# Kernel optimization log

Measured on AMD Instinct MI355X. Metric: run time of the kernel, lower is better.

## Reference

```python
import jax, jax.numpy as jnp
import numpy as np

N, M, D_IN, D_TXT, D_OUT, H = 4096, 1024, 512, 512, 512, 8
DH = D_OUT // H


def positional_encoding(n, dim):
    # Matches PositionalEncoding: freq = exp((arange(dim//2)/dim)*ln(10000)),
    # x = pos/freq -> [L, dim//2], interleave (sin, cos) pairs -> [L, dim].
    pos = jnp.arange(n, dtype=jnp.float32)
    freq = jnp.exp((jnp.arange(dim // 2, dtype=jnp.float32) / dim) * jnp.log(jnp.float32(10000.0)))
    x = pos[:, None] / freq  # [L, dim//2]
    pe = jnp.stack((jnp.sin(x), jnp.cos(x)), axis=-1)  # [L, dim//2, 2]
    return pe.reshape(n, dim)


def setup_inputs() -> dict:
    key = jax.random.key(0)
    k1, k2, k3, k4, k5, k6 = jax.random.split(key, 6)
    s = 0.02
    return {
        "video_features": jax.random.normal(k1, (N, D_IN), dtype=jnp.float32),
        "text_features": jax.random.normal(k2, (M, D_TXT), dtype=jnp.float32),
        "Wq": jax.random.normal(k3, (H, D_IN, DH), dtype=jnp.float32) * s,
        "Wk": jax.random.normal(k4, (H, D_TXT, DH), dtype=jnp.float32) * s,
        "Wv": jax.random.normal(k5, (H, D_TXT, DH), dtype=jnp.float32) * s,
        "Wout": jax.random.normal(k6, (D_OUT, D_IN), dtype=jnp.float32) * s,
    }


def reference(video_features, text_features, Wq, Wk, Wv, Wout):
    # Batched over heads instead of the original per-head Python loop (same math).
    Q = jnp.einsum('nd,hde->hne', video_features, Wq)   # [H, N, DH]
    K = jnp.einsum('md,hde->hme', text_features, Wk)    # [H, M, DH]
    V = jnp.einsum('md,hde->hme', text_features, Wv)    # [H, M, DH]
    energies = jnp.einsum('hne,hme->hnm', Q, K)         # no scaling in original
    att = jax.nn.softmax(energies, axis=-1)             # dropout omitted (eval mode)
    y = jnp.einsum('hnm,hme->hne', att, V)              # [H, N, DH]
    y = jnp.transpose(y, (1, 0, 2)).reshape(video_features.shape[0], -1)  # concat heads
    y = y @ Wout                                        # [N, D_IN]
    y = y + positional_encoding(y.shape[0], y.shape[1])
    return y
```

## Files before the change

kernel.cpp:

```cpp
#include <hip/hip_runtime.h>
#include <hip/hip_bf16.h>
#include <math.h>

#define N_TOK 4096
#define M_TOK 1024
#define DMODEL 512
#define NHEAD 8
#define DHEAD 64

typedef __attribute__((ext_vector_type(8))) short short8;
typedef __attribute__((ext_vector_type(4))) float f32x4;
typedef __attribute__((ext_vector_type(4))) float float4v;
typedef __attribute__((ext_vector_type(2))) float float2v;

static __device__ __forceinline__ short f2bf(float f) {
    union { float f; unsigned u; } v; v.f = f;
    unsigned r = v.u + 0x7fffu + ((v.u >> 16) & 1u);
    return (short)(r >> 16);
}

#define GLOAD_LDS16(g, l) __builtin_amdgcn_global_load_lds( \
    (const __attribute__((address_space(1))) void*)(g), \
    (__attribute__((address_space(3))) void*)(l), 16, 0, 0)

__global__ void pack_kernel(const float* __restrict__ xv, const float* __restrict__ xt,
                            const float* __restrict__ wq, const float* __restrict__ wk,
                            const float* __restrict__ wv, const float* __restrict__ wo,
                            short* __restrict__ xvb, short* __restrict__ xtb,
                            short* __restrict__ wqb, short* __restrict__ wkb,
                            short* __restrict__ wvb, short* __restrict__ wob,
                            float* __restrict__ pe) {
    int idx = blockIdx.x * 256 + threadIdx.x;
    int stride = gridDim.x * 256;
    const int CXV = N_TOK * DMODEL / 8;
    const int CXT = M_TOK * DMODEL / 8;
    const int NW  = DMODEL * DMODEL;
    const int NPE = N_TOK * (DMODEL / 2);
    for (int c = idx; c < CXV; c += stride) {
        float4v f0 = *(const float4v*)&xv[c * 8];
        float4v f1 = *(const float4v*)&xv[c * 8 + 4];
        short8 o;
        #pragma unroll
        for (int j = 0; j < 4; j++) { o[j] = f2bf(f0[j]); o[j + 4] = f2bf(f1[j]); }
        *(short8*)&xvb[c * 8] = o;
    }
    for (int c = idx; c < CXT; c += stride) {
        float4v f0 = *(const float4v*)&xt[c * 8];
        float4v f1 = *(const float4v*)&xt[c * 8 + 4];
        short8 o;
        #pragma unroll
        for (int j = 0; j < 4; j++) { o[j] = f2bf(f0[j]); o[j + 4] = f2bf(f1[j]); }
        *(short8*)&xtb[c * 8] = o;
    }
    for (int i = idx; i < NW; i += stride) {
        int n = i >> 9;
        int k = i & 511;
        int h = n >> 6, e = n & 63;
        int src = h * (DMODEL * DHEAD) + k * DHEAD + e;
        wqb[i] = f2bf(wq[src]);
        wkb[i] = f2bf(wk[src]);
        wvb[i] = f2bf(wv[src]);
        wob[i] = f2bf(wo[k * DMODEL + n]);
    }
    for (int i = idx; i < NPE; i += stride) {
        int row = i >> 8;
        int p = i & 255;
        float fr = __expf(-(float)p * (9.210340371976184f / 512.0f));
        float x = (float)row * fr;
        float s, c;
        __sincosf(x, &s, &c);
        float2v sc; sc[0] = s; sc[1] = c;
        *(float2v*)&pe[(size_t)row * DMODEL + p * 2] = sc;
    }
}

template<typename EPI>
static __device__ __forceinline__ void gemm_body(const short* __restrict__ A,
                                                 const short* __restrict__ BT,
                                                 int m0, int n0, EPI epi) {
    __shared__ __align__(16) short As[64][72];
    __shared__ __align__(16) short Bs[64][72];
    int t = threadIdx.x;
    int lane = t & 63, w = t >> 6;
    int wr = w >> 1, wc = w & 1;
    int l15 = lane & 15, g = lane >> 4;

    int row = t >> 2, c0 = (t & 3) * 16;
    const short* gA = A + (size_t)(m0 + row) * DMODEL + c0;
    const short* gB = BT + (size_t)(n0 + row) * DMODEL + c0;

    short8 ra0 = *(const short8*)gA;
    short8 ra1 = *(const short8*)(gA + 8);
    short8 rb0 = *(const short8*)gB;
    short8 rb1 = *(const short8*)(gB + 8);

    f32x4 acc[2][2] = {};
    #pragma unroll
    for (int step = 0; step < DMODEL / 64; ++step) {
        *(short8*)&As[row][c0]     = ra0;
        *(short8*)&As[row][c0 + 8] = ra1;
        *(short8*)&Bs[row][c0]     = rb0;
        *(short8*)&Bs[row][c0 + 8] = rb1;
        __syncthreads();
        if (step < DMODEL / 64 - 1) {
            gA += 64; gB += 64;
            ra0 = *(const short8*)gA;
            ra1 = *(const short8*)(gA + 8);
            rb0 = *(const short8*)gB;
            rb1 = *(const short8*)(gB + 8);
        }
        #pragma unroll
        for (int ks = 0; ks < 2; ks++) {
            short8 a[2], b[2];
            #pragma unroll
            for (int fr = 0; fr < 2; fr++) a[fr] = *(short8*)&As[wr * 32 + fr * 16 + l15][ks * 32 + g * 8];
            #pragma unroll
            for (int fc = 0; fc < 2; fc++) b[fc] = *(short8*)&Bs[wc * 32 + fc * 16 + l15][ks * 32 + g * 8];
            #pragma unroll
            for (int fr = 0; fr < 2; fr++)
                #pragma unroll
                for (int fc = 0; fc < 2; fc++)
                    acc[fr][fc] = __builtin_amdgcn_mfma_f32_16x16x32_bf16(a[fr], b[fc], acc[fr][fc], 0, 0, 0);
        }
        __syncthreads();
    }
    #pragma unroll
    for (int fr = 0; fr < 2; fr++)
        #pragma unroll
        for (int fc = 0; fc < 2; fc++)
            #pragma unroll
            for (int r = 0; r < 4; r++) {
                int orow = m0 + wr * 32 + fr * 16 + g * 4 + r;
                int ocol = n0 + wc * 32 + fc * 16 + l15;
                epi(orow, ocol, acc[fr][fc][r]);
            }
}

__global__ __launch_bounds__(256) void gemmQKV(const short* __restrict__ xvb,
                                               const short* __restrict__ xtb,
                                               const short* __restrict__ wqb,
                                               const short* __restrict__ wkb,
                                               const short* __restrict__ wvb,
                                               short* __restrict__ qb,
                                               short* __restrict__ kbm,
                                               short* __restrict__ vbt) {
    int bx = blockIdx.x;
    int n0 = blockIdx.y * 64;
    if (bx < 64) {
        short* C = qb;
        gemm_body(xvb, wqb, bx * 64, n0,
                  [&](int row, int col, float v) { C[(size_t)row * DMODEL + col] = f2bf(v); });
    } else if (bx < 80) {
        short* C = kbm;
        gemm_body(xtb, wkb, (bx - 64) * 64, n0,
                  [&](int row, int col, float v) { C[(size_t)row * DMODEL + col] = f2bf(v); });
    } else {
        short* C = vbt;
        gemm_body(xtb, wvb, (bx - 80) * 64, n0,
                  [&](int row, int col, float v) { C[(size_t)col * M_TOK + row] = f2bf(v); });
    }
}

__global__ __launch_bounds__(256) void gemmOut(const short* __restrict__ A,
                                               const short* __restrict__ BT,
                                               const float* __restrict__ pe,
                                               float* __restrict__ Cout) {
    gemm_body(A, BT, blockIdx.x * 64, blockIdx.y * 64,
              [&](int row, int col, float v) {
                  size_t o = (size_t)row * DMODEL + col;
                  Cout[o] = v + pe[o];
              });
}

__global__ __launch_bounds__(256) void attn_kernel(const short* __restrict__ Qb,
                                                   const short* __restrict__ Kb,
                                                   const short* __restrict__ VbT,
                                                   short* __restrict__ Yb) {
    __shared__ __align__(16) short Ks[2][64][64];
    __shared__ __align__(16) short Vs[2][64][64];
    __shared__ __align__(16) short Ps[4][16][72];

    int bid = blockIdx.x;
    int h = bid & 7;
    int qx = bid >> 3;
    int n0 = qx * 64;
    int t = threadIdx.x;
    int lane = t & 63, w = t >> 6;
    int l15 = lane & 15, g = lane >> 4;

    const short* Kh  = Kb + h * DHEAD;
    const short* VhT = VbT + (h * DHEAD) * M_TOK;

    int srow = (lane >> 3);
    int sgran = (lane & 7) ^ srow;
    const short* gK0 = Kh + (size_t)(w * 16 + srow) * DMODEL + sgran * 8;
    const short* gV0 = VhT + (size_t)(w * 16 + srow) * M_TOK + sgran * 8;

    const short* qrow = Qb + (size_t)(n0 + w * 16 + l15) * DMODEL + h * DHEAD;
    short8 qa0 = *(const short8*)(qrow + g * 8);
    short8 qa1 = *(const short8*)(qrow + 32 + g * 8);

    f32x4 acc[4] = {};
    f32x4 rsum = {};
    int sx = l15 & 7;

    {
        GLOAD_LDS16(gK0,                 &Ks[0][w * 16][0]);
        GLOAD_LDS16(gK0 + 8 * DMODEL,    &Ks[0][w * 16 + 8][0]);
        GLOAD_LDS16(gV0,                 &Vs[0][w * 16][0]);
        GLOAD_LDS16(gV0 + 8 * M_TOK,     &Vs[0][w * 16 + 8][0]);
    }
    __syncthreads();

    int buf = 0;
    for (int it = 0; it < 16; ++it) {
        if (it < 15) {
            int key0 = (it + 1) * 64;
            GLOAD_LDS16(gK0 + (size_t)key0 * DMODEL,             &Ks[buf ^ 1][w * 16][0]);
            GLOAD_LDS16(gK0 + (size_t)(key0 + 8) * DMODEL,       &Ks[buf ^ 1][w * 16 + 8][0]);
            GLOAD_LDS16(gV0 + key0,                              &Vs[buf ^ 1][w * 16][0]);
            GLOAD_LDS16(gV0 + key0 + 8 * M_TOK,                  &Vs[buf ^ 1][w * 16 + 8][0]);
        }
        #pragma unroll
        for (int kt = 0; kt < 4; kt++) {
            short8 kf0 = *(short8*)&Ks[buf][kt * 16 + l15][((g) ^ sx) * 8];
            short8 kf1 = *(short8*)&Ks[buf][kt * 16 + l15][((4 + g) ^ sx) * 8];
            f32x4 e = {};
            e = __builtin_amdgcn_mfma_f32_16x16x32_bf16(qa0, kf0, e, 0, 0, 0);
            e = __builtin_amdgcn_mfma_f32_16x16x32_bf16(qa1, kf1, e, 0, 0, 0);
            #pragma unroll
            for (int r = 0; r < 4; r++) {
                float p = exp2f(e[r] * 1.44269504f);
                rsum[r] += p;
                Ps[w][g * 4 + r][kt * 16 + l15] = f2bf(p);
            }
        }
        #pragma unroll
        for (int kb2 = 0; kb2 < 2; kb2++) {
            short8 pa = *(short8*)&Ps[w][l15][kb2 * 32 + g * 8];
            #pragma unroll
            for (int nt = 0; nt < 4; nt++) {
                short8 vf = *(short8*)&Vs[buf][nt * 16 + l15][((kb2 * 4 + g) ^ sx) * 8];
                acc[nt] = __builtin_amdgcn_mfma_f32_16x16x32_bf16(pa, vf, acc[nt], 0, 0, 0);
            }
        }
        __syncthreads();
        buf ^= 1;
    }

    #pragma unroll
    for (int r = 0; r < 4; r++) {
        float s = rsum[r];
        s += __shfl_xor(s, 1);
        s += __shfl_xor(s, 2);
        s += __shfl_xor(s, 4);
        s += __shfl_xor(s, 8);
        rsum[r] = s;
    }

    #pragma unroll
    for (int nt = 0; nt < 4; nt++)
        #pragma unroll
        for (int r = 0; r < 4; r++) {
            float y = acc[nt][r] / rsum[r];
            Yb[(size_t)(n0 + w * 16 + g * 4 + r) * DMODEL + h * DHEAD + nt * 16 + l15] = f2bf(y);
        }
}

extern "C" void kernel_launch(void* const* d_in, const int* in_sizes, int n_in,
                              void* d_out, int out_size, void* d_ws, size_t ws_size,
                              hipStream_t stream) {
    const float* xv = (const float*)d_in[0];
    const float* xt = (const float*)d_in[1];
    const float* wq = (const float*)d_in[2];
    const float* wk = (const float*)d_in[3];
    const float* wv = (const float*)d_in[4];
    const float* wo = (const float*)d_in[5];

    short* xvb = (short*)d_ws;
    short* xtb = xvb + N_TOK * DMODEL;
    short* wqb = xtb + M_TOK * DMODEL;
    short* wkb = wqb + DMODEL * DMODEL;
    short* wvb = wkb + DMODEL * DMODEL;
    short* wob = wvb + DMODEL * DMODEL;
    short* qb  = wob + DMODEL * DMODEL;
    short* kbm = qb  + N_TOK * DMODEL;
    short* vbt = kbm + M_TOK * DMODEL;
    short* yb  = vbt + M_TOK * DMODEL;
    float* pe  = (float*)(yb + N_TOK * DMODEL);

    pack_kernel<<<1024, 256, 0, stream>>>(xv, xt, wq, wk, wv, wo,
                                          xvb, xtb, wqb, wkb, wvb, wob, pe);
    gemmQKV<<<dim3(96, 8), 256, 0, stream>>>(xvb, xtb, wqb, wkb, wvb, qb, kbm, vbt);
    attn_kernel<<<512, 256, 0, stream>>>(qb, kbm, vbt, yb);
    gemmOut<<<dim3(64, 8), 256, 0, stream>>>(yb, wob, pe, (float*)d_out);
}
```

Measured before the change: 62.65 us.

## Fuse QKV, attention and output GEMMs into persistent kernel with grid barriers

Replaces three separate launches (QKV GEMM, attention, output GEMM) with a single 512-block kernel that runs each stage in turn, separated by a software grid barrier built on global atomics, with shared memory reused through a union. The positional encoding is now computed inline in the output GEMM epilogue rather than being materialised by the pack kernel and read back. This removes launch gaps and the PE write/read traffic, but it depends on all 512 blocks being co-resident for the barrier. It also loses parallelism in the QKV stage, where half the blocks compute two tiles.

```diff
diff --git a/kernel.cpp b/kernel.cpp
--- a/kernel.cpp
+++ b/kernel.cpp
@@ -7,11 +7,11 @@
 #define DMODEL 512
 #define NHEAD 8
 #define DHEAD 64
+#define NBLK 512
 
 typedef __attribute__((ext_vector_type(8))) short short8;
 typedef __attribute__((ext_vector_type(4))) float f32x4;
 typedef __attribute__((ext_vector_type(4))) float float4v;
-typedef __attribute__((ext_vector_type(2))) float float2v;
 
 static __device__ __forceinline__ short f2bf(float f) {
     union { float f; unsigned u; } v; v.f = f;
@@ -22,6 +22,29 @@
 #define GLOAD_LDS16(g, l) __builtin_amdgcn_global_load_lds( \
     (const __attribute__((address_space(1))) void*)(g), \
     (__attribute__((address_space(3))) void*)(l), 16, 0, 0)
+
+struct SMemG { short As[64][72]; short Bs[64][72]; };
+struct SMemA { short Ks[2][64][64]; short Vs[2][64][64]; short Ps[4][16][72]; };
+union SMemU { SMemG g; SMemA a; };
+
+static __device__ __forceinline__ void gridbar(unsigned* cnt, unsigned* gen) {
+    __syncthreads();
+    if (threadIdx.x == 0) {
+        __threadfence();
+        unsigned g = __hip_atomic_load(gen, __ATOMIC_RELAXED, __HIP_MEMORY_SCOPE_AGENT);
+        if (__hip_atomic_fetch_add(cnt, 1u, __ATOMIC_ACQ_REL, __HIP_MEMORY_SCOPE_AGENT) == NBLK - 1u) {
+            __hip_atomic_store(cnt, 0u, __ATOMIC_RELAXED, __HIP_MEMORY_SCOPE_AGENT);
+            __hip_atomic_store(gen, g + 1u, __ATOMIC_RELEASE, __HIP_MEMORY_SCOPE_AGENT);
+        } else {
+            unsigned cur;
+            do {
+                __builtin_amdgcn_s_sleep(2);
+                cur = __hip_atomic_load(gen, __ATOMIC_ACQUIRE, __HIP_MEMORY_SCOPE_AGENT);
+            } while (cur == g);
+        }
+    }
+    __syncthreads();
+}
 
 __global__ void pack_kernel(const float* __restrict__ xv, const float* __restrict__ xt,
                             const float* __restrict__ wq, const float* __restrict__ wk,
@@ -29,13 +52,13 @@
                             short* __restrict__ xvb, short* __restrict__ xtb,
                             short* __restrict__ wqb, short* __restrict__ wkb,
                             short* __restrict__ wvb, short* __restrict__ wob,
-                            float* __restrict__ pe) {
+                            unsigned* __restrict__ bar) {
     int idx = blockIdx.x * 256 + threadIdx.x;
     int stride = gridDim.x * 256;
+    if (idx == 0) { bar[0] = 0u; bar[1] = 0u; }
     const int CXV = N_TOK * DMODEL / 8;
     const int CXT = M_TOK * DMODEL / 8;
     const int NW  = DMODEL * DMODEL;
-    const int NPE = N_TOK * (DMODEL / 2);
     for (int c = idx; c < CXV; c += stride) {
         float4v f0 = *(const float4v*)&xv[c * 8];
         float4v f1 = *(const float4v*)&xv[c * 8 + 4];
@@ -62,24 +85,13 @@
         wvb[i] = f2bf(wv[src]);
         wob[i] = f2bf(wo[k * DMODEL + n]);
     }
-    for (int i = idx; i < NPE; i += stride) {
-        int row = i >> 8;
-        int p = i & 255;
-        float fr = __expf(-(float)p * (9.210340371976184f / 512.0f));
-        float x = (float)row * fr;
-        float s, c;
-        __sincosf(x, &s, &c);
-        float2v sc; sc[0] = s; sc[1] = c;
-        *(float2v*)&pe[(size_t)row * DMODEL + p * 2] = sc;
-    }
 }
 
 template<typename EPI>
-static __device__ __forceinline__ void gemm_body(const short* __restrict__ A,
+static __device__ __forceinline__ void gemm_body(SMemG& sm,
+                                                 const short* __restrict__ A,
                                                  const short* __restrict__ BT,
                                                  int m0, int n0, EPI epi) {
-    __shared__ __align__(16) short As[64][72];
-    __shared__ __align__(16) short Bs[64][72];
     int t = threadIdx.x;
     int lane = t & 63, w = t >> 6;
     int wr = w >> 1, wc = w & 1;
@@ -97,10 +109,10 @@
     f32x4 acc[2][2] = {};
     #pragma unroll
     for (int step = 0; step < DMODEL / 64; ++step) {
-        *(short8*)&As[row][c0]     = ra0;
-        *(short8*)&As[row][c0 + 8] = ra1;
-        *(short8*)&Bs[row][c0]     = rb0;
-        *(short8*)&Bs[row][c0 + 8] = rb1;
+        *(short8*)&sm.As[row][c0]     = ra0;
+        *(short8*)&sm.As[row][c0 + 8] = ra1;
+        *(short8*)&sm.Bs[row][c0]     = rb0;
+        *(short8*)&sm.Bs[row][c0 + 8] = rb1;
         __syncthreads();
         if (step < DMODEL / 64 - 1) {
             gA += 64; gB += 64;
@@ -113,9 +125,9 @@
         for (int ks = 0; ks < 2; ks++) {
             short8 a[2], b[2];
             #pragma unroll
-            for (int fr = 0; fr < 2; fr++) a[fr] = *(short8*)&As[wr * 32 + fr * 16 + l15][ks * 32 + g * 8];
-            #pragma unroll
-            for (int fc = 0; fc < 2; fc++) b[fc] = *(short8*)&Bs[wc * 32 + fc * 16 + l15][ks * 32 + g * 8];
+            for (int fr = 0; fr < 2; fr++) a[fr] = *(short8*)&sm.As[wr * 32 + fr * 16 + l15][ks * 32 + g * 8];
+            #pragma unroll
+            for (int fc = 0; fc < 2; fc++) b[fc] = *(short8*)&sm.Bs[wc * 32 + fc * 16 + l15][ks * 32 + g * 8];
             #pragma unroll
             for (int fr = 0; fr < 2; fr++)
                 #pragma unroll
@@ -136,54 +148,32 @@
             }
 }
 
-__global__ __launch_bounds__(256) void gemmQKV(const short* __restrict__ xvb,
-                                               const short* __restrict__ xtb,
-                                               const short* __restrict__ wqb,
-                                               const short* __restrict__ wkb,
-                                               const short* __restrict__ wvb,
-                                               short* __restrict__ qb,
-                                               short* __restrict__ kbm,
-                                               short* __restrict__ vbt) {
-    int bx = blockIdx.x;
-    int n0 = blockIdx.y * 64;
-    if (bx < 64) {
-        short* C = qb;
-        gemm_body(xvb, wqb, bx * 64, n0,
-                  [&](int row, int col, float v) { C[(size_t)row * DMODEL + col] = f2bf(v); });
-    } else if (bx < 80) {
-        short* C = kbm;
-        gemm_body(xtb, wkb, (bx - 64) * 64, n0,
-                  [&](int row, int col, float v) { C[(size_t)row * DMODEL + col] = f2bf(v); });
+static __device__ __forceinline__ void qkv_tile(SMemG& sm, int tile,
+                                                const short* xvb, const short* xtb,
+                                                const short* wqb, const short* wkb,
+                                                const short* wvb,
+                                                short* qb, short* kbm, short* vbt) {
+    if (tile < 512) {
+        gemm_body(sm, xvb, wqb, (tile >> 3) * 64, (tile & 7) * 64,
+                  [&](int row, int col, float v) { qb[(size_t)row * DMODEL + col] = f2bf(v); });
+    } else if (tile < 640) {
+        int b = tile - 512;
+        gemm_body(sm, xtb, wkb, (b >> 3) * 64, (b & 7) * 64,
+                  [&](int row, int col, float v) { kbm[(size_t)row * DMODEL + col] = f2bf(v); });
     } else {
-        short* C = vbt;
-        gemm_body(xtb, wvb, (bx - 80) * 64, n0,
-                  [&](int row, int col, float v) { C[(size_t)col * M_TOK + row] = f2bf(v); });
-    }
-}
-
-__global__ __launch_bounds__(256) void gemmOut(const short* __restrict__ A,
-                                               const short* __restrict__ BT,
-                                               const float* __restrict__ pe,
-                                               float* __restrict__ Cout) {
-    gemm_body(A, BT, blockIdx.x * 64, blockIdx.y * 64,
-              [&](int row, int col, float v) {
-                  size_t o = (size_t)row * DMODEL + col;
-                  Cout[o] = v + pe[o];
-              });
-}
-
-__global__ __launch_bounds__(256) void attn_kernel(const short* __restrict__ Qb,
-                                                   const short* __restrict__ Kb,
-                                                   const short* __restrict__ VbT,
-                                                   short* __restrict__ Yb) {
-    __shared__ __align__(16) short Ks[2][64][64];
-    __shared__ __align__(16) short Vs[2][64][64];
-    __shared__ __align__(16) short Ps[4][16][72];
-
-    int bid = blockIdx.x;
+        int b = tile - 640;
+        gemm_body(sm, xtb, wvb, (b >> 3) * 64, (b & 7) * 64,
+                  [&](int row, int col, float v) { vbt[(size_t)col * M_TOK + row] = f2bf(v); });
+    }
+}
+
+static __device__ __forceinline__ void attn_tile(SMemA& sm, int bid,
+                                                 const short* __restrict__ Qb,
+                                                 const short* __restrict__ Kb,
+                                                 const short* __restrict__ VbT,
+                                                 short* __restrict__ Yb) {
     int h = bid & 7;
-    int qx = bid >> 3;
-    int n0 = qx * 64;
+    int n0 = (bid >> 3) * 64;
     int t = threadIdx.x;
     int lane = t & 63, w = t >> 6;
     int l15 = lane & 15, g = lane >> 4;
@@ -204,27 +194,25 @@
     f32x4 rsum = {};
     int sx = l15 & 7;
 
-    {
-        GLOAD_LDS16(gK0,                 &Ks[0][w * 16][0]);
-        GLOAD_LDS16(gK0 + 8 * DMODEL,    &Ks[0][w * 16 + 8][0]);
-        GLOAD_LDS16(gV0,                 &Vs[0][w * 16][0]);
-        GLOAD_LDS16(gV0 + 8 * M_TOK,     &Vs[0][w * 16 + 8][0]);
-    }
+    GLOAD_LDS16(gK0,              &sm.Ks[0][w * 16][0]);
+    GLOAD_LDS16(gK0 + 8 * DMODEL, &sm.Ks[0][w * 16 + 8][0]);
+    GLOAD_LDS16(gV0,              &sm.Vs[0][w * 16][0]);
+    GLOAD_LDS16(gV0 + 8 * M_TOK,  &sm.Vs[0][w * 16 + 8][0]);
     __syncthreads();
 
     int buf = 0;
     for (int it = 0; it < 16; ++it) {
         if (it < 15) {
             int key0 = (it + 1) * 64;
-            GLOAD_LDS16(gK0 + (size_t)key0 * DMODEL,             &Ks[buf ^ 1][w * 16][0]);
-            GLOAD_LDS16(gK0 + (size_t)(key0 + 8) * DMODEL,       &Ks[buf ^ 1][w * 16 + 8][0]);
-            GLOAD_LDS16(gV0 + key0,                              &Vs[buf ^ 1][w * 16][0]);
-            GLOAD_LDS16(gV0 + key0 + 8 * M_TOK,                  &Vs[buf ^ 1][w * 16 + 8][0]);
+            GLOAD_LDS16(gK0 + (size_t)key0 * DMODEL,       &sm.Ks[buf ^ 1][w * 16][0]);
+            GLOAD_LDS16(gK0 + (size_t)(key0 + 8) * DMODEL, &sm.Ks[buf ^ 1][w * 16 + 8][0]);
+            GLOAD_LDS16(gV0 + key0,                        &sm.Vs[buf ^ 1][w * 16][0]);
+            GLOAD_LDS16(gV0 + key0 + 8 * M_TOK,            &sm.Vs[buf ^ 1][w * 16 + 8][0]);
         }
         #pragma unroll
         for (int kt = 0; kt < 4; kt++) {
-            short8 kf0 = *(short8*)&Ks[buf][kt * 16 + l15][((g) ^ sx) * 8];
-            short8 kf1 = *(short8*)&Ks[buf][kt * 16 + l15][((4 + g) ^ sx) * 8];
+            short8 kf0 = *(short8*)&sm.Ks[buf][kt * 16 + l15][((g) ^ sx) * 8];
+            short8 kf1 = *(short8*)&sm.Ks[buf][kt * 16 + l15][((4 + g) ^ sx) * 8];
             f32x4 e = {};
             e = __builtin_amdgcn_mfma_f32_16x16x32_bf16(qa0, kf0, e, 0, 0, 0);
             e = __builtin_amdgcn_mfma_f32_16x16x32_bf16(qa1, kf1, e, 0, 0, 0);
@@ -232,15 +220,15 @@
             for (int r = 0; r < 4; r++) {
                 float p = exp2f(e[r] * 1.44269504f);
                 rsum[r] += p;
-                Ps[w][g * 4 + r][kt * 16 + l15] = f2bf(p);
+                sm.Ps[w][g * 4 + r][kt * 16 + l15] = f2bf(p);
             }
         }
         #pragma unroll
         for (int kb2 = 0; kb2 < 2; kb2++) {
-            short8 pa = *(short8*)&Ps[w][l15][kb2 * 32 + g * 8];
+            short8 pa = *(short8*)&sm.Ps[w][l15][kb2 * 32 + g * 8];
             #pragma unroll
             for (int nt = 0; nt < 4; nt++) {
-                short8 vf = *(short8*)&Vs[buf][nt * 16 + l15][((kb2 * 4 + g) ^ sx) * 8];
+                short8 vf = *(short8*)&sm.Vs[buf][nt * 16 + l15][((kb2 * 4 + g) ^ sx) * 8];
                 acc[nt] = __builtin_amdgcn_mfma_f32_16x16x32_bf16(pa, vf, acc[nt], 0, 0, 0);
             }
         }
@@ -265,6 +253,37 @@
             float y = acc[nt][r] / rsum[r];
             Yb[(size_t)(n0 + w * 16 + g * 4 + r) * DMODEL + h * DHEAD + nt * 16 + l15] = f2bf(y);
         }
+}
+
+__global__ __launch_bounds__(256) void mega_kernel(const short* xvb, const short* xtb,
+                                                   const short* wqb, const short* wkb,
+                                                   const short* wvb, const short* wob,
+                                                   short* qb, short* kbm, short* vbt,
+                                                   short* yb, float* outp,
+                                                   unsigned* bar) {
+    __shared__ SMemU sm;
+    __shared__ float ifreq[256];
+    int t = threadIdx.x;
+    ifreq[t] = __expf(-(float)t * (9.210340371976184f / 512.0f));
+    int bx = blockIdx.x;
+
+    qkv_tile(sm.g, bx, xvb, xtb, wqb, wkb, wvb, qb, kbm, vbt);
+    if (bx < 256) {
+        __syncthreads();
+        qkv_tile(sm.g, 512 + bx, xvb, xtb, wqb, wkb, wvb, qb, kbm, vbt);
+    }
+    gridbar(&bar[0], &bar[1]);
+
+    attn_tile(sm.a, bx, qb, kbm, vbt, yb);
+    gridbar(&bar[0], &bar[1]);
+
+    gemm_body(sm.g, yb, wob, (bx >> 3) * 64, (bx & 7) * 64,
+              [&](int row, int col, float v) {
+                  float x = (float)row * ifreq[col >> 1];
+                  float s, c;
+                  __sincosf(x, &s, &c);
+                  outp[(size_t)row * DMODEL + col] = v + ((col & 1) ? c : s);
+              });
 }
 
 extern "C" void kernel_launch(void* const* d_in, const int* in_sizes, int n_in,
@@ -287,11 +306,10 @@
     short* kbm = qb  + N_TOK * DMODEL;
     short* vbt = kbm + M_TOK * DMODEL;
     short* yb  = vbt + M_TOK * DMODEL;
-    float* pe  = (float*)(yb + N_TOK * DMODEL);
+    unsigned* bar = (unsigned*)(yb + N_TOK * DMODEL);
 
     pack_kernel<<<1024, 256, 0, stream>>>(xv, xt, wq, wk, wv, wo,
-                                          xvb, xtb, wqb, wkb, wvb, wob, pe);
-    gemmQKV<<<dim3(96, 8), 256, 0, stream>>>(xvb, xtb, wqb, wkb, wvb, qb, kbm, vbt);
-    attn_kernel<<<512, 256, 0, stream>>>(qb, kbm, vbt, yb);
-    gemmOut<<<dim3(64, 8), 256, 0, stream>>>(yb, wob, pe, (float*)d_out);
-}
+                                          xvb, xtb, wqb, wkb, wvb, wob, bar);
+    mega_kernel<<<NBLK, 256, 0, stream>>>(xvb, xtb, wqb, wkb, wvb, wob,
+                                          qb, kbm, vbt, yb, (float*)d_out, bar);
+}
```

New measurement: 209.8 us. +234.9%, slower.

## Tile weight transposes through LDS and compute positional encoding in output epilogue

Applied to the files above, without the earlier changes.

Weight packing is rewritten so dedicated blocks transpose 64x64 tiles through shared memory, which gives coalesced reads and writes in place of strided scalar gathers. The positional-encoding table is no longer written to and read back from global memory. Instead, gemmOut computes sin/cos inline in its epilogue using per-block inverse frequencies held in LDS. This removes about 8 MB of PE traffic and the uncoalesced weight accesses, at the cost of extra transcendental math in the GEMM epilogue.

```diff
diff --git a/kernel.cpp b/kernel.cpp
--- a/kernel.cpp
+++ b/kernel.cpp
@@ -11,7 +11,6 @@
 typedef __attribute__((ext_vector_type(8))) short short8;
 typedef __attribute__((ext_vector_type(4))) float f32x4;
 typedef __attribute__((ext_vector_type(4))) float float4v;
-typedef __attribute__((ext_vector_type(2))) float float2v;
 
 static __device__ __forceinline__ short f2bf(float f) {
     union { float f; unsigned u; } v; v.f = f;
@@ -23,19 +22,71 @@
     (const __attribute__((address_space(1))) void*)(g), \
     (__attribute__((address_space(3))) void*)(l), 16, 0, 0)
 
-__global__ void pack_kernel(const float* __restrict__ xv, const float* __restrict__ xt,
-                            const float* __restrict__ wq, const float* __restrict__ wk,
-                            const float* __restrict__ wv, const float* __restrict__ wo,
-                            short* __restrict__ xvb, short* __restrict__ xtb,
-                            short* __restrict__ wqb, short* __restrict__ wkb,
-                            short* __restrict__ wvb, short* __restrict__ wob,
-                            float* __restrict__ pe) {
-    int idx = blockIdx.x * 256 + threadIdx.x;
-    int stride = gridDim.x * 256;
+__global__ __launch_bounds__(256) void pack_kernel(
+        const float* __restrict__ xv, const float* __restrict__ xt,
+        const float* __restrict__ wq, const float* __restrict__ wk,
+        const float* __restrict__ wv, const float* __restrict__ wo,
+        short* __restrict__ xvb, short* __restrict__ xtb,
+        short* __restrict__ wqb, short* __restrict__ wkb,
+        short* __restrict__ wvb, short* __restrict__ wob) {
+    int bid = blockIdx.x;
+    int t = threadIdx.x;
+    if (bid < 256) {
+        __shared__ float lds[64][65];
+        const float* src;
+        short* dst;
+        int srstride;
+        int dr0, dc0;
+        if (bid < 192) {
+            int mat = bid >> 6;
+            int hb = bid & 63;
+            int h = hb >> 3, dt = hb & 7;
+            const float* W = (mat == 0) ? wq : (mat == 1) ? wk : wv;
+            src = W + (size_t)h * (DMODEL * DHEAD) + (size_t)(dt * 64) * DHEAD;
+            srstride = DHEAD;
+            dst = (mat == 0) ? wqb : (mat == 1) ? wkb : wvb;
+            dr0 = h * 64;
+            dc0 = dt * 64;
+        } else {
+            int b = bid - 192;
+            int rt = b >> 3, ct = b & 7;
+            src = wo + (size_t)(rt * 64) * DMODEL + ct * 64;
+            srstride = DMODEL;
+            dst = wob;
+            dr0 = ct * 64;
+            dc0 = rt * 64;
+        }
+        {
+            int r = t >> 2, c0 = (t & 3) * 16;
+            const float* s = src + (size_t)r * srstride + c0;
+            #pragma unroll
+            for (int j = 0; j < 4; j++) {
+                float4v v = *(const float4v*)(s + j * 4);
+                lds[r][c0 + j * 4 + 0] = v[0];
+                lds[r][c0 + j * 4 + 1] = v[1];
+                lds[r][c0 + j * 4 + 2] = v[2];
+                lds[r][c0 + j * 4 + 3] = v[3];
+            }
+        }
+        __syncthreads();
+        {
+            int outr = t >> 2, c0 = (t & 3) * 16;
+            short8 o0, o1;
+            #pragma unroll
+            for (int j = 0; j < 8; j++) {
+                o0[j] = f2bf(lds[c0 + j][outr]);
+                o1[j] = f2bf(lds[c0 + 8 + j][outr]);
+            }
+            short* d = dst + (size_t)(dr0 + outr) * DMODEL + dc0 + c0;
+            *(short8*)d = o0;
+            *(short8*)(d + 8) = o1;
+        }
+        return;
+    }
+    int idx = (bid - 256) * 256 + t;
+    int stride = (gridDim.x - 256) * 256;
     const int CXV = N_TOK * DMODEL / 8;
     const int CXT = M_TOK * DMODEL / 8;
-    const int NW  = DMODEL * DMODEL;
-    const int NPE = N_TOK * (DMODEL / 2);
     for (int c = idx; c < CXV; c += stride) {
         float4v f0 = *(const float4v*)&xv[c * 8];
         float4v f1 = *(const float4v*)&xv[c * 8 + 4];
@@ -51,26 +102,6 @@
         #pragma unroll
         for (int j = 0; j < 4; j++) { o[j] = f2bf(f0[j]); o[j + 4] = f2bf(f1[j]); }
         *(short8*)&xtb[c * 8] = o;
-    }
-    for (int i = idx; i < NW; i += stride) {
-        int n = i >> 9;
-        int k = i & 511;
-        int h = n >> 6, e = n & 63;
-        int src = h * (DMODEL * DHEAD) + k * DHEAD + e;
-        wqb[i] = f2bf(wq[src]);
-        wkb[i] = f2bf(wk[src]);
-        wvb[i] = f2bf(wv[src]);
-        wob[i] = f2bf(wo[k * DMODEL + n]);
-    }
-    for (int i = idx; i < NPE; i += stride) {
-        int row = i >> 8;
-        int p = i & 255;
-        float fr = __expf(-(float)p * (9.210340371976184f / 512.0f));
-        float x = (float)row * fr;
-        float s, c;
-        __sincosf(x, &s, &c);
-        float2v sc; sc[0] = s; sc[1] = c;
-        *(float2v*)&pe[(size_t)row * DMODEL + p * 2] = sc;
     }
 }
 
@@ -163,12 +194,16 @@
 
 __global__ __launch_bounds__(256) void gemmOut(const short* __restrict__ A,
                                                const short* __restrict__ BT,
-                                               const float* __restrict__ pe,
                                                float* __restrict__ Cout) {
+    __shared__ float ifreq[256];
+    ifreq[threadIdx.x] = __expf(-(float)threadIdx.x * (9.210340371976184f / 512.0f));
+    __syncthreads();
     gemm_body(A, BT, blockIdx.x * 64, blockIdx.y * 64,
               [&](int row, int col, float v) {
-                  size_t o = (size_t)row * DMODEL + col;
-                  Cout[o] = v + pe[o];
+                  float x = (float)row * ifreq[col >> 1];
+                  float s, c;
+                  __sincosf(x, &s, &c);
+                  Cout[(size_t)row * DMODEL + col] = v + ((col & 1) ? c : s);
               });
 }
 
@@ -182,8 +217,7 @@
 
     int bid = blockIdx.x;
     int h = bid & 7;
-    int qx = bid >> 3;
-    int n0 = qx * 64;
+    int n0 = (bid >> 3) * 64;
     int t = threadIdx.x;
     int lane = t & 63, w = t >> 6;
     int l15 = lane & 15, g = lane >> 4;
@@ -204,22 +238,20 @@
     f32x4 rsum = {};
     int sx = l15 & 7;
 
-    {
-        GLOAD_LDS16(gK0,                 &Ks[0][w * 16][0]);
-        GLOAD_LDS16(gK0 + 8 * DMODEL,    &Ks[0][w * 16 + 8][0]);
-        GLOAD_LDS16(gV0,                 &Vs[0][w * 16][0]);
-        GLOAD_LDS16(gV0 + 8 * M_TOK,     &Vs[0][w * 16 + 8][0]);
-    }
+    GLOAD_LDS16(gK0,              &Ks[0][w * 16][0]);
+    GLOAD_LDS16(gK0 + 8 * DMODEL, &Ks[0][w * 16 + 8][0]);
+    GLOAD_LDS16(gV0,              &Vs[0][w * 16][0]);
+    GLOAD_LDS16(gV0 + 8 * M_TOK,  &Vs[0][w * 16 + 8][0]);
     __syncthreads();
 
     int buf = 0;
     for (int it = 0; it < 16; ++it) {
         if (it < 15) {
             int key0 = (it + 1) * 64;
-            GLOAD_LDS16(gK0 + (size_t)key0 * DMODEL,             &Ks[buf ^ 1][w * 16][0]);
-            GLOAD_LDS16(gK0 + (size_t)(key0 + 8) * DMODEL,       &Ks[buf ^ 1][w * 16 + 8][0]);
-            GLOAD_LDS16(gV0 + key0,                              &Vs[buf ^ 1][w * 16][0]);
-            GLOAD_LDS16(gV0 + key0 + 8 * M_TOK,                  &Vs[buf ^ 1][w * 16 + 8][0]);
+            GLOAD_LDS16(gK0 + (size_t)key0 * DMODEL,       &Ks[buf ^ 1][w * 16][0]);
+            GLOAD_LDS16(gK0 + (size_t)(key0 + 8) * DMODEL, &Ks[buf ^ 1][w * 16 + 8][0]);
+            GLOAD_LDS16(gV0 + key0,                        &Vs[buf ^ 1][w * 16][0]);
+            GLOAD_LDS16(gV0 + key0 + 8 * M_TOK,            &Vs[buf ^ 1][w * 16 + 8][0]);
         }
         #pragma unroll
         for (int kt = 0; kt < 4; kt++) {
@@ -287,11 +319,10 @@
     short* kbm = qb  + N_TOK * DMODEL;
     short* vbt = kbm + M_TOK * DMODEL;
     short* yb  = vbt + M_TOK * DMODEL;
-    float* pe  = (float*)(yb + N_TOK * DMODEL);
-
-    pack_kernel<<<1024, 256, 0, stream>>>(xv, xt, wq, wk, wv, wo,
-                                          xvb, xtb, wqb, wkb, wvb, wob, pe);
+
+    pack_kernel<<<1280, 256, 0, stream>>>(xv, xt, wq, wk, wv, wo,
+                                          xvb, xtb, wqb, wkb, wvb, wob);
     gemmQKV<<<dim3(96, 8), 256, 0, stream>>>(xvb, xtb, wqb, wkb, wvb, qb, kbm, vbt);
     attn_kernel<<<512, 256, 0, stream>>>(qb, kbm, vbt, yb);
-    gemmOut<<<dim3(64, 8), 256, 0, stream>>>(yb, wob, pe, (float*)d_out);
-}
+    gemmOut<<<dim3(64, 8), 256, 0, stream>>>(yb, wob, (float*)d_out);
+}
```

After: 58.45 us. -6.7%, faster.
